# Kernel tuning notes

Hardware: AMD Instinct MI355X
Metric: run time of the kernel (lower is better)

## Reference

```python
import jax, jax.numpy as jnp
import numpy as np

N_NODES = 100000
HIDDEN = 128
N_EDGES = 640000


def setup_inputs() -> dict:
    key = jax.random.key(0)
    ks = jax.random.split(key, 9)
    X = jax.random.normal(ks[0], (N_NODES, HIDDEN), dtype=jnp.float32)
    edge_index = jax.random.randint(ks[1], (2, N_EDGES), 0, N_NODES, dtype=jnp.int64)
    s = 1.0 / np.sqrt(HIDDEN)
    W_in = jax.random.uniform(ks[2], (HIDDEN, HIDDEN), jnp.float32, -s, s)
    b_in = jax.random.uniform(ks[3], (HIDDEN,), jnp.float32, -s, s)
    W_gate = jax.random.uniform(ks[4], (HIDDEN, HIDDEN), jnp.float32, -s, s)
    b_gate = jax.random.uniform(ks[5], (HIDDEN,), jnp.float32, -s, s)
    W_out = jax.random.uniform(ks[6], (HIDDEN, HIDDEN), jnp.float32, -s, s)
    b_out = jax.random.uniform(ks[7], (HIDDEN,), jnp.float32, -s, s)
    return {"X": X, "edge_index": edge_index, "W_in": W_in, "b_in": b_in,
            "W_gate": W_gate, "b_gate": b_gate, "W_out": W_out, "b_out": b_out}


def reference(X, edge_index, W_in, b_in, W_gate, b_gate, W_out, b_out):
    src = edge_index[0]
    dst = edge_index[1]
    n = X.shape[0]
    # gather messages from source nodes, scatter-add into destinations
    messages = X[src]  # [E, d]
    agg = jax.ops.segment_sum(messages, dst, num_segments=n)  # [N, d]
    deg = jax.ops.segment_sum(jnp.ones_like(dst, dtype=X.dtype), dst, num_segments=n)
    deg = jnp.clip(deg, 1.0, None)[:, None]  # [N, 1]
    agg = agg / deg
    # gated MLP (torch Linear: x @ W.T + b)
    h = agg @ W_in.T + b_in
    g = jax.nn.sigmoid(agg @ W_gate.T + b_gate)
    out = (jax.nn.relu(h) * g) @ W_out.T + b_out
    return out
```

## Files before the change

### kernel.cpp

```cpp
#include <hip/hip_runtime.h>
#include <hip/hip_bf16.h>

#define HID 128
#define CAP 32
#define CSTRIDE 16

typedef __attribute__((ext_vector_type(8))) __bf16 bf16x8;
typedef __attribute__((ext_vector_type(4))) float f32x4;
typedef __attribute__((ext_vector_type(8))) unsigned short us8;

__device__ __forceinline__ unsigned short f2bf(float f){
  unsigned int u = __float_as_uint(f);
  unsigned int r = (u + 0x7FFFu + ((u >> 16) & 1u)) >> 16;
  return (unsigned short)r;
}

__global__ void mega_kernel(const float* __restrict__ X, uint2* __restrict__ Xb, int n4,
                            const int* __restrict__ ei, int* __restrict__ cntp,
                            int* __restrict__ ell, int E, int nFillBlk,
                            const float* __restrict__ Win, const float* __restrict__ Wg,
                            const float* __restrict__ Wo, unsigned short* __restrict__ wfrag,
                            int N){
  int b = blockIdx.x;
  if (b < nFillBlk){
    int e = b*256 + threadIdx.x;
    if (e >= E) return;
    int s = ei[e], d = ei[E + e];
    int slot = atomicAdd(&cntp[d*CSTRIDE], 1);
    if (slot < CAP) ell[((size_t)d << 5) + slot] = s;
    return;
  }
  b -= nFillBlk;
  if (b < 24){
    int f = b*256 + threadIdx.x;
    if (f >= 3*2048) return;
    int m = f >> 11, fi = f & 2047;
    int l = fi & 63, nfks = fi >> 6, ks = nfks & 3, nf = nfks >> 2;
    const float* W = (m == 0) ? Win : ((m == 1) ? Wg : Wo);
    int row = nf*16 + (l & 15), k0 = ks*32 + ((l >> 4) << 3);
    float4 a = *(const float4*)(W + row*HID + k0);
    float4 bb = *(const float4*)(W + row*HID + k0 + 4);
    us8 o = { f2bf(a.x), f2bf(a.y), f2bf(a.z), f2bf(a.w),
              f2bf(bb.x), f2bf(bb.y), f2bf(bb.z), f2bf(bb.w) };
    *(us8*)(wfrag + (size_t)f*8) = o;
    return;
  }
  b -= 24;
  int i = b*256 + threadIdx.x;
  if (i < n4){
    float4 v = ((const float4*)X)[i];
    uint2 o;
    o.x = (unsigned)f2bf(v.x) | ((unsigned)f2bf(v.y) << 16);
    o.y = (unsigned)f2bf(v.z) | ((unsigned)f2bf(v.w) << 16);
    Xb[i] = o;
  }
  if (i < 32){ uint2 z; z.x = 0u; z.y = 0u; Xb[n4 + i] = z; }
}

__global__ __launch_bounds__(256) void gather_kernel(const uint2* __restrict__ Xu2,
                              const int* __restrict__ ell, const int* __restrict__ cntp,
                              uint2* __restrict__ agg2, int N){
  int wv = threadIdx.x >> 6, lane = threadIdx.x & 63;
  int h = lane >> 5, cl = lane & 31;
  int n = blockIdx.x*8 + wv*2 + h;
  bool valid = (n < N);
  int nn = valid ? n : N-1;
  int d = cntp[nn*CSTRIDE];
  int dd = (d < CAP) ? d : CAP;
  int m = dd - 1;
  int mc = (m < 0) ? 0 : m;
  int le = (cl < mc) ? cl : mc;
  int sp = (dd > 0) ? ell[((size_t)nn << 5) + le] : N;
  int ddo = __shfl_xor(dd, 32);
  int dmax = (dd > ddo) ? dd : ddo;
  float a0 = 0.f, a1 = 0.f, a2 = 0.f, a3 = 0.f;
  for (int j = 0; j < dmax; j += 4){
    uint2 p[4];
    #pragma unroll
    for (int u = 0; u < 4; ++u){
      int jj = j + u;
      int js = (jj < mc) ? jj : mc;
      int s = __shfl(sp, (h << 5) + js);
      s = (jj <= m) ? s : N;
      p[u] = Xu2[(unsigned)s*32u + cl];
    }
    #pragma unroll
    for (int u = 0; u < 4; ++u){
      a0 += __uint_as_float(p[u].x << 16);
      a1 += __uint_as_float(p[u].x & 0xFFFF0000u);
      a2 += __uint_as_float(p[u].y << 16);
      a3 += __uint_as_float(p[u].y & 0xFFFF0000u);
    }
  }
  if (valid){
    float inv = (d > 0) ? 1.f/(float)d : 0.f;
    uint2 o;
    o.x = (unsigned)f2bf(a0*inv) | ((unsigned)f2bf(a1*inv) << 16);
    o.y = (unsigned)f2bf(a2*inv) | ((unsigned)f2bf(a3*inv) << 16);
    agg2[(unsigned)n*32u + cl] = o;
  }
}

__global__ __launch_bounds__(512, 4) void mlp_kernel(const unsigned short* __restrict__ aggb,
    const unsigned short* __restrict__ wfrag,
    const float* __restrict__ bin, const float* __restrict__ bg, const float* __restrict__ bo,
    float* __restrict__ out, int N){
  __shared__ unsigned short s_w[2*16384];
  __shared__ float s_bias[3*HID];
  const int tid = threadIdx.x;
  const int n0 = blockIdx.x * 128;

  for (int i = tid; i < 4096; i += 512)
    ((us8*)s_w)[i] = ((const us8*)wfrag)[i];
  if (tid < 3*HID){
    const float* bsrc = (tid < HID) ? bin : ((tid < 2*HID) ? bg : bo);
    s_bias[tid] = bsrc[tid & (HID-1)];
  }
  __syncthreads();

  const int l  = tid & 63;
  const int wv = tid >> 6;
  const int r0 = wv * 16;
  const int kq = (l >> 4) * 8;

  int arow = n0 + r0 + (l & 15); if (arow > N-1) arow = N-1;
  bf16x8 afr[4];
  #pragma unroll
  for (int ks = 0; ks < 4; ++ks)
    afr[ks] = *(const bf16x8*)(aggb + (size_t)arow*HID + ks*32 + kq);

  f32x4 acch[8], accg[8];
  #pragma unroll
  for (int nf = 0; nf < 8; ++nf){ acch[nf] = {0.f,0.f,0.f,0.f}; accg[nf] = {0.f,0.f,0.f,0.f}; }

  #pragma unroll
  for (int nf = 0; nf < 8; ++nf){
    #pragma unroll
    for (int ks = 0; ks < 4; ++ks){
      const int fb = ((nf*4 + ks)*64 + l) * 8;
      bf16x8 b1 = *(const bf16x8*)(s_w + fb);
      bf16x8 b2 = *(const bf16x8*)(s_w + 16384 + fb);
      acch[nf] = __builtin_amdgcn_mfma_f32_16x16x32_bf16(afr[ks], b1, acch[nf], 0, 0, 0);
      accg[nf] = __builtin_amdgcn_mfma_f32_16x16x32_bf16(afr[ks], b2, accg[nf], 0, 0, 0);
    }
  }

  __syncthreads();

  unsigned short* tw = s_w + 16384 + wv*2048;
  const int rrb = (l >> 4) * 4;
  #pragma unroll
  for (int nf = 0; nf < 8; ++nf){
    const int c = nf*16 + (l & 15);
    const int ks2 = c >> 5, sub = (c >> 3) & 3, e = c & 7;
    const float bi = s_bias[c], bgv = s_bias[HID + c];
    #pragma unroll
    for (int rg = 0; rg < 4; ++rg){
      float hh = acch[nf][rg] + bi;
      float gg = accg[nf][rg] + bgv;
      float t = fmaxf(hh, 0.f) * (1.f / (1.f + __expf(-gg)));
      int blk = sub*16 + rrb + rg;
      blk ^= (blk >> 4) & 3;
      tw[ks2*512 + blk*8 + e] = f2bf(t);
    }
  }

  bf16x8 tfr[4];
  #pragma unroll
  for (int ks = 0; ks < 4; ++ks)
    tfr[ks] = *(const bf16x8*)(tw + ks*512 + (size_t)(l ^ ((l >> 4) & 3))*8);

  f32x4 acco[8];
  #pragma unroll
  for (int nf = 0; nf < 8; ++nf) acco[nf] = {0.f,0.f,0.f,0.f};
  #pragma unroll
  for (int nf = 0; nf < 8; ++nf){
    #pragma unroll
    for (int ks = 0; ks < 4; ++ks){
      const int fb = ((nf*4 + ks)*64 + l) * 8;
      bf16x8 b3 = *(const bf16x8*)(wfrag + 32768 + fb);
      acco[nf] = __builtin_amdgcn_mfma_f32_16x16x32_bf16(tfr[ks], b3, acco[nf], 0, 0, 0);
    }
  }
  #pragma unroll
  for (int nf = 0; nf < 8; ++nf){
    const int c = nf*16 + (l & 15);
    const float bov = s_bias[2*HID + c];
    #pragma unroll
    for (int rg = 0; rg < 4; ++rg){
      int node = n0 + r0 + rrb + rg;
      if (node < N) out[(size_t)node*HID + c] = acco[nf][rg] + bov;
    }
  }
}

extern "C" void kernel_launch(void* const* d_in, const int* in_sizes, int n_in,
                              void* d_out, int out_size, void* d_ws, size_t ws_size,
                              hipStream_t stream){
  const float* X   = (const float*)d_in[0];
  const int*   ei  = (const int*)d_in[1];
  const float* Win = (const float*)d_in[2];
  const float* bin = (const float*)d_in[3];
  const float* Wg  = (const float*)d_in[4];
  const float* bg  = (const float*)d_in[5];
  const float* Wo  = (const float*)d_in[6];
  const float* bo  = (const float*)d_in[7];
  float* out = (float*)d_out;
  const int N = in_sizes[0] / HID;
  const int E = in_sizes[1] / 2;

  unsigned short* Xb    = (unsigned short*)d_ws;
  unsigned short* agg   = Xb + (size_t)(N+1)*HID;
  unsigned short* wfrag = agg + (size_t)N*HID;
  int* cntp = (int*)(wfrag + 3*16384);
  int* ell  = cntp + (size_t)N*CSTRIDE;

  const int n4 = N*HID/4;
  const int nFillBlk = (E + 255)/256;
  const int nConvBlk = (n4 + 255)/256;
  hipMemsetAsync(cntp, 0, (size_t)N*CSTRIDE*sizeof(int), stream);
  mega_kernel  <<<nFillBlk + 24 + nConvBlk, 256, 0, stream>>>(X, (uint2*)Xb, n4, ei, cntp,
                                                              ell, E, nFillBlk,
                                                              Win, Wg, Wo, wfrag, N);
  gather_kernel<<<(N + 7)/8, 256, 0, stream>>>((const uint2*)Xb, ell, cntp,
                                               (uint2*)agg, N);
  mlp_kernel   <<<(N + 127)/128, 512, 0, stream>>>(agg, wfrag, bin, bg, bo, out, N);
}
```

Measured before the change: 108.6 us.

## Pack per-node degree and neighbor list into one record with overflow list

Stores each node's degree counter and up to 15 neighbor indices in a single 64-byte record, instead of a padded counter array plus a separate 32-slot ELL array. Edges beyond 15 per node go to a global overflow list of (dst, src) pairs. Each gather thread now reads one cache line per node for both the count and the neighbors, and the scatter writes also land in that line, cutting memory traffic. The cost is that rare high-degree nodes must linearly scan the overflow list, and a second atomic counter is contended on overflow.

```diff
diff --git a/kernel.cpp b/kernel.cpp
--- a/kernel.cpp
+++ b/kernel.cpp
@@ -2,8 +2,8 @@
 #include <hip/hip_bf16.h>
 
 #define HID 128
-#define CAP 32
-#define CSTRIDE 16
+#define CAP 15
+#define OVFMAX 16384
 
 typedef __attribute__((ext_vector_type(8))) __bf16 bf16x8;
 typedef __attribute__((ext_vector_type(4))) float f32x4;
@@ -16,8 +16,9 @@
 }
 
 __global__ void mega_kernel(const float* __restrict__ X, uint2* __restrict__ Xb, int n4,
-                            const int* __restrict__ ei, int* __restrict__ cntp,
-                            int* __restrict__ ell, int E, int nFillBlk,
+                            const int* __restrict__ ei, unsigned int* __restrict__ rec,
+                            unsigned int* __restrict__ ovfc, uint2* __restrict__ ovf,
+                            int E, int nFillBlk,
                             const float* __restrict__ Win, const float* __restrict__ Wg,
                             const float* __restrict__ Wo, unsigned short* __restrict__ wfrag,
                             int N){
@@ -26,8 +27,13 @@
     int e = b*256 + threadIdx.x;
     if (e >= E) return;
     int s = ei[e], d = ei[E + e];
-    int slot = atomicAdd(&cntp[d*CSTRIDE], 1);
-    if (slot < CAP) ell[((size_t)d << 5) + slot] = s;
+    unsigned slot = atomicAdd(&rec[(unsigned)d*16u], 1u);
+    if (slot < CAP){
+      rec[(unsigned)d*16u + 1u + slot] = (unsigned)s;
+    } else {
+      unsigned k = atomicAdd(ovfc, 1u);
+      if (k < OVFMAX){ uint2 pr; pr.x = (unsigned)d; pr.y = (unsigned)s; ovf[k] = pr; }
+    }
     return;
   }
   b -= nFillBlk;
@@ -58,30 +64,27 @@
 }
 
 __global__ __launch_bounds__(256) void gather_kernel(const uint2* __restrict__ Xu2,
-                              const int* __restrict__ ell, const int* __restrict__ cntp,
+                              const unsigned int* __restrict__ rec,
+                              const unsigned int* __restrict__ ovfc,
+                              const uint2* __restrict__ ovf,
                               uint2* __restrict__ agg2, int N){
   int wv = threadIdx.x >> 6, lane = threadIdx.x & 63;
   int h = lane >> 5, cl = lane & 31;
   int n = blockIdx.x*8 + wv*2 + h;
   bool valid = (n < N);
   int nn = valid ? n : N-1;
-  int d = cntp[nn*CSTRIDE];
+  unsigned r = rec[(unsigned)nn*16u + (cl & 15)];
+  int d = (int)__shfl((int)r, (h << 5));
   int dd = (d < CAP) ? d : CAP;
-  int m = dd - 1;
-  int mc = (m < 0) ? 0 : m;
-  int le = (cl < mc) ? cl : mc;
-  int sp = (dd > 0) ? ell[((size_t)nn << 5) + le] : N;
-  int ddo = __shfl_xor(dd, 32);
-  int dmax = (dd > ddo) ? dd : ddo;
   float a0 = 0.f, a1 = 0.f, a2 = 0.f, a3 = 0.f;
-  for (int j = 0; j < dmax; j += 4){
+  for (int j = 0; j < dd; j += 4){
     uint2 p[4];
     #pragma unroll
     for (int u = 0; u < 4; ++u){
       int jj = j + u;
-      int js = (jj < mc) ? jj : mc;
-      int s = __shfl(sp, (h << 5) + js);
-      s = (jj <= m) ? s : N;
+      int js = (jj < dd) ? jj : 0;
+      int s = (int)__shfl((int)r, (h << 5) + 1 + js);
+      s = (jj < dd) ? s : N;
       p[u] = Xu2[(unsigned)s*32u + cl];
     }
     #pragma unroll
@@ -90,6 +93,19 @@
       a1 += __uint_as_float(p[u].x & 0xFFFF0000u);
       a2 += __uint_as_float(p[u].y << 16);
       a3 += __uint_as_float(p[u].y & 0xFFFF0000u);
+    }
+  }
+  if (d > CAP){
+    int oc = (int)*ovfc; if (oc > OVFMAX) oc = OVFMAX;
+    for (int i = 0; i < oc; ++i){
+      uint2 e = ovf[i];
+      if ((int)e.x == nn){
+        uint2 p = Xu2[(size_t)e.y*32u + cl];
+        a0 += __uint_as_float(p.x << 16);
+        a1 += __uint_as_float(p.x & 0xFFFF0000u);
+        a2 += __uint_as_float(p.y << 16);
+        a3 += __uint_as_float(p.y & 0xFFFF0000u);
+      }
     }
   }
   if (valid){
@@ -212,17 +228,18 @@
   unsigned short* Xb    = (unsigned short*)d_ws;
   unsigned short* agg   = Xb + (size_t)(N+1)*HID;
   unsigned short* wfrag = agg + (size_t)N*HID;
-  int* cntp = (int*)(wfrag + 3*16384);
-  int* ell  = cntp + (size_t)N*CSTRIDE;
+  unsigned int* rec  = (unsigned int*)(wfrag + 3*16384);
+  unsigned int* ovfc = rec + (size_t)N*16;
+  uint2* ovf = (uint2*)(ovfc + 16);
 
   const int n4 = N*HID/4;
   const int nFillBlk = (E + 255)/256;
   const int nConvBlk = (n4 + 255)/256;
-  hipMemsetAsync(cntp, 0, (size_t)N*CSTRIDE*sizeof(int), stream);
-  mega_kernel  <<<nFillBlk + 24 + nConvBlk, 256, 0, stream>>>(X, (uint2*)Xb, n4, ei, cntp,
-                                                              ell, E, nFillBlk,
+  hipMemsetAsync(rec, 0, ((size_t)N*16 + 16)*sizeof(unsigned int), stream);
+  mega_kernel  <<<nFillBlk + 24 + nConvBlk, 256, 0, stream>>>(X, (uint2*)Xb, n4, ei, rec,
+                                                              ovfc, ovf, E, nFillBlk,
                                                               Win, Wg, Wo, wfrag, N);
-  gather_kernel<<<(N + 7)/8, 256, 0, stream>>>((const uint2*)Xb, ell, cntp,
+  gather_kernel<<<(N + 7)/8, 256, 0, stream>>>((const uint2*)Xb, rec, ovfc, ovf,
                                                (uint2*)agg, N);
   mlp_kernel   <<<(N + 127)/128, 512, 0, stream>>>(agg, wfrag, bin, bg, bo, out, N);
 }
```

Result: slower. 118.6 us (+9.3%).

## Partition edge bucketing by destination range per XCD and compact degree counters

Applied to the files above, without the earlier changes.

The edge-fill phase now launches eight blocks per edge chunk. Each block reads the destination indices and handles only the edges whose destination falls in the node range assigned to its XCD (block index mod 8). The aim is to keep the atomic counters and ELL writes local to one XCD's L2 and avoid cross-die coherence traffic. The padded per-node counter stride of 16 ints is replaced by a dense int array, which shrinks the memset and the counter reads in the gather kernel. The cost is eight times as many fill blocks and reads of the destination array, and the gain relies on the hardware mapping blocks round-robin onto XCDs.

```diff
diff --git a/kernel.cpp b/kernel.cpp
--- a/kernel.cpp
+++ b/kernel.cpp
@@ -3,7 +3,6 @@
 
 #define HID 128
 #define CAP 32
-#define CSTRIDE 16
 
 typedef __attribute__((ext_vector_type(8))) __bf16 bf16x8;
 typedef __attribute__((ext_vector_type(4))) float f32x4;
@@ -16,18 +15,24 @@
 }
 
 __global__ void mega_kernel(const float* __restrict__ X, uint2* __restrict__ Xb, int n4,
-                            const int* __restrict__ ei, int* __restrict__ cntp,
-                            int* __restrict__ ell, int E, int nFillBlk,
+                            const int* __restrict__ ei, int* __restrict__ cnt,
+                            int* __restrict__ ell, int E, int nFillBlk, int n8,
                             const float* __restrict__ Win, const float* __restrict__ Wg,
                             const float* __restrict__ Wo, unsigned short* __restrict__ wfrag,
                             int N){
   int b = blockIdx.x;
   if (b < nFillBlk){
-    int e = b*256 + threadIdx.x;
-    if (e >= E) return;
-    int s = ei[e], d = ei[E + e];
-    int slot = atomicAdd(&cntp[d*CSTRIDE], 1);
-    if (slot < CAP) ell[((size_t)d << 5) + slot] = s;
+    int chunk = b >> 3;
+    unsigned xcd = (unsigned)(b & 7);
+    int e = chunk*256 + threadIdx.x;
+    if (e < E){
+      int d = ei[E + e];
+      if ((unsigned)d / (unsigned)n8 == xcd){
+        int s = ei[e];
+        int slot = atomicAdd(&cnt[d], 1);
+        if (slot < CAP) ell[((size_t)d << 5) + slot] = s;
+      }
+    }
     return;
   }
   b -= nFillBlk;
@@ -58,14 +63,14 @@
 }
 
 __global__ __launch_bounds__(256) void gather_kernel(const uint2* __restrict__ Xu2,
-                              const int* __restrict__ ell, const int* __restrict__ cntp,
+                              const int* __restrict__ ell, const int* __restrict__ cnt,
                               uint2* __restrict__ agg2, int N){
   int wv = threadIdx.x >> 6, lane = threadIdx.x & 63;
   int h = lane >> 5, cl = lane & 31;
   int n = blockIdx.x*8 + wv*2 + h;
   bool valid = (n < N);
   int nn = valid ? n : N-1;
-  int d = cntp[nn*CSTRIDE];
+  int d = cnt[nn];
   int dd = (d < CAP) ? d : CAP;
   int m = dd - 1;
   int mc = (m < 0) ? 0 : m;
@@ -212,17 +217,18 @@
   unsigned short* Xb    = (unsigned short*)d_ws;
   unsigned short* agg   = Xb + (size_t)(N+1)*HID;
   unsigned short* wfrag = agg + (size_t)N*HID;
-  int* cntp = (int*)(wfrag + 3*16384);
-  int* ell  = cntp + (size_t)N*CSTRIDE;
+  int* cnt = (int*)(wfrag + 3*16384);
+  int* ell = cnt + N;
 
   const int n4 = N*HID/4;
-  const int nFillBlk = (E + 255)/256;
+  const int n8 = (N + 7)/8;
+  const int nFillBlk = ((E + 255)/256)*8;
   const int nConvBlk = (n4 + 255)/256;
-  hipMemsetAsync(cntp, 0, (size_t)N*CSTRIDE*sizeof(int), stream);
-  mega_kernel  <<<nFillBlk + 24 + nConvBlk, 256, 0, stream>>>(X, (uint2*)Xb, n4, ei, cntp,
-                                                              ell, E, nFillBlk,
+  hipMemsetAsync(cnt, 0, (size_t)N*sizeof(int), stream);
+  mega_kernel  <<<nFillBlk + 24 + nConvBlk, 256, 0, stream>>>(X, (uint2*)Xb, n4, ei, cnt,
+                                                              ell, E, nFillBlk, n8,
                                                               Win, Wg, Wo, wfrag, N);
-  gather_kernel<<<(N + 7)/8, 256, 0, stream>>>((const uint2*)Xb, ell, cntp,
+  gather_kernel<<<(N + 7)/8, 256, 0, stream>>>((const uint2*)Xb, ell, cnt,
                                                (uint2*)agg, N);
   mlp_kernel   <<<(N + 127)/128, 512, 0, stream>>>(agg, wfrag, bin, bg, bo, out, N);
 }
```

After: 107.2 us. No clear change (-1.3%).
